# Performance work log

Measured on AMD Instinct MI355X. Metric: run time of the kernel, lower is better.

Reference implementation:

```python
import jax, jax.numpy as jnp
import numpy as np

NUM_HEADS = 16


def setup_inputs() -> dict:
    key = jax.random.key(0)
    k0, k1, k2, k3 = jax.random.split(key, 4)
    B, N, C = 8, 1024, 1024
    D = C // NUM_HEADS
    x = jax.random.normal(k0, (B, N, C), dtype=jnp.float32)
    # RoPE angle table [1, N, 1, head_dim]
    rope_freqs = jax.random.uniform(k1, (1, N, 1, D), dtype=jnp.float32) * (2.0 * jnp.pi)
    # qkv: Linear(dim, 3*dim, bias=False); proj: Linear(dim, dim) with bias
    qkv_w = jax.random.normal(k2, (3 * C, C), dtype=jnp.float32) * 0.02
    proj_w = jax.random.normal(k3, (C, C), dtype=jnp.float32) * 0.02
    proj_b = jnp.zeros((C,), dtype=jnp.float32)
    return {"x": x, "rope_freqs": rope_freqs, "qkv_w": qkv_w, "proj_w": proj_w, "proj_b": proj_b}


def _rotate_half(t):
    t1, t2 = jnp.split(t, 2, axis=-1)
    return jnp.concatenate([-t2, t1], axis=-1)


def reference(x, rope_freqs, qkv_w, proj_w, proj_b):
    B, N, C = x.shape
    H = NUM_HEADS
    D = C // H
    scale = D ** (-0.5)
    # QKV projection -> [3, B, H, N, D]
    qkv = (x @ qkv_w.T).reshape(B, N, 3, H, D).transpose(2, 0, 3, 1, 4)
    q, k, v = qkv[0], qkv[1], qkv[2]
    # RoPE: freqs [1, N, 1, D] -> [1, 1, N, D], applied to all tokens (n_special = 0)
    freqs = jnp.transpose(rope_freqs, (0, 2, 1, 3))
    cos = jnp.cos(freqs).astype(q.dtype)
    sin = jnp.sin(freqs).astype(q.dtype)
    q = q * cos + _rotate_half(q) * sin
    k = k * cos + _rotate_half(k) * sin
    # Full materialized attention (as in source)
    attn = jax.nn.softmax(jnp.einsum("bhnd,bhmd->bhnm", q, k) * scale, axis=-1)
    out = jnp.einsum("bhnm,bhmd->bhnd", attn, v)  # [B, H, N, D]
    out = out.transpose(0, 2, 1, 3).reshape(B, N, C)
    return out @ proj_w.T + proj_b
```

## Files before the change

### kernel.cpp

```cpp
#include <hip/hip_runtime.h>


typedef __attribute__((ext_vector_type(8))) short bf16x8;
typedef __attribute__((ext_vector_type(4))) float floatx4;
typedef __attribute__((ext_vector_type(4))) unsigned int u32x4;
typedef __attribute__((ext_vector_type(2))) unsigned int u32x2;

__device__ __forceinline__ void gld16(const void* g, void* l) {
  __builtin_amdgcn_global_load_lds((const __attribute__((address_space(1))) void*)g,
                                   (__attribute__((address_space(3))) void*)l, 16, 0, 0);
}

__device__ __forceinline__ short f2bf(float f) {
  unsigned u = __builtin_bit_cast(unsigned, f);
  u = (u + 0x7FFFu + ((u >> 16) & 1u)) >> 16;
  return (short)u;
}
__device__ __forceinline__ unsigned cvtpk(float lo, float hi) {
  unsigned r;
  asm("v_cvt_pk_bf16_f32 %0, %1, %2" : "=v"(r) : "v"(lo), "v"(hi));
  return r;
}
__device__ __forceinline__ float pexp(float x) {
  float r;
  asm("v_exp_f32 %0, %1" : "=v"(r) : "v"(x));
  return r;
}

__global__ __launch_bounds__(256) void prep_all(const float* __restrict__ sx,
                                                const float* __restrict__ sq,
                                                const float* __restrict__ sp,
                                                short* __restrict__ dst,
                                                const float* __restrict__ ropef,
                                                float2* __restrict__ tbl) {
  int bid = blockIdx.x;
  if (bid < 12288) {
    int i = bid * 256 + threadIdx.x;
    const float4* src;
    if (i < 2097152)      src = reinterpret_cast<const float4*>(sx) + i;
    else if (i < 2883584) src = reinterpret_cast<const float4*>(sq) + (i - 2097152);
    else                  src = reinterpret_cast<const float4*>(sp) + (i - 2883584);
    float4 v = *src;
    short4 o;
    o.x = f2bf(v.x); o.y = f2bf(v.y); o.z = f2bf(v.z); o.w = f2bf(v.w);
    reinterpret_cast<short4*>(dst)[i] = o;
  } else {
    int i = (bid - 12288) * 256 + threadIdx.x;
    float v = ropef[i];
    tbl[i] = make_float2(cosf(v), sinf(v));
  }
}

#define QSCALE 0.18033688011112042f

__device__ __forceinline__ void gemm_main(const short* __restrict__ A,
                                          const short* __restrict__ Bm,
                                          short* As, short* Bs,
                                          floatx4 (&acc)[2][4],
                                          int bx, int by) {
  const int tid = threadIdx.x;
  const int wid = tid >> 6, lane = tid & 63;
  const int g = lane >> 4, l15 = lane & 15;
  const int wr = wid >> 2, wc = wid & 3;
  const size_t trow = (size_t)by * 128, tcol = (size_t)bx * 256;
  floatx4 zero = {0.f, 0.f, 0.f, 0.f};
  #pragma unroll
  for (int i = 0; i < 2; ++i)
    #pragma unroll
    for (int j = 0; j < 4; ++j) acc[i][j] = zero;

  auto stage = [&](int buf, int k0) {
    {
      const int cb = wid * 64;
      const int c  = cb + lane;
      const int r  = c >> 3, s = c & 7;
      const int koff = k0 + ((s ^ (r & 7)) << 3);
      gld16(A + (trow + r) * 1024 + koff, As + buf * 8192 + (size_t)cb * 8);
    }
    #pragma unroll
    for (int i = 0; i < 2; ++i) {
      const int cb = (i * 16 + wid) * 64;
      const int c  = cb + lane;
      const int r  = c >> 3, s = c & 7;
      const int koff = k0 + ((s ^ (r & 7)) << 3);
      gld16(Bm + (tcol + r) * 1024 + koff, Bs + buf * 16384 + (size_t)cb * 8);
    }
  };

  stage(0, 0);
  __syncthreads();

  for (int t = 0; t < 16; ++t) {
    const int buf = t & 1;
    if (t < 15) stage(buf ^ 1, (t + 1) * 64);
    const short* Ab = As + buf * 8192;
    const short* Bb = Bs + buf * 16384;
    #pragma unroll
    for (int ks = 0; ks < 2; ++ks) {
      bf16x8 af[2], bfr[4];
      #pragma unroll
      for (int mi = 0; mi < 2; ++mi) {
        int row = wr * 32 + mi * 16 + l15;
        int ch  = (ks * 4 + g) ^ (row & 7);
        af[mi] = *reinterpret_cast<const bf16x8*>(Ab + row * 64 + ch * 8);
      }
      #pragma unroll
      for (int nt = 0; nt < 4; ++nt) {
        int row = wc * 64 + nt * 16 + l15;
        int ch  = (ks * 4 + g) ^ (row & 7);
        bfr[nt] = *reinterpret_cast<const bf16x8*>(Bb + row * 64 + ch * 8);
      }
      __builtin_amdgcn_s_setprio(1);
      #pragma unroll
      for (int mi = 0; mi < 2; ++mi)
        #pragma unroll
        for (int nt = 0; nt < 4; ++nt)
          acc[mi][nt] = __builtin_amdgcn_mfma_f32_16x16x32_bf16(af[mi], bfr[nt],
                                                                acc[mi][nt], 0, 0, 0);
      __builtin_amdgcn_s_setprio(0);
    }
    __syncthreads();
  }
}

__global__ __launch_bounds__(1024, 4) void gemm_qkv_k(const short* __restrict__ A,
                                                      const short* __restrict__ Bm,
                                                      const float2* __restrict__ tbl,
                                                      short* __restrict__ qo,
                                                      short* __restrict__ ko,
                                                      short* __restrict__ vt) {
  extern __shared__ __align__(16) short smem[];
  short* As = smem;
  short* Bs = smem + 16384;
  const int id  = blockIdx.y * 12 + blockIdx.x;
  const int sid = (id & 7) * 96 + (id >> 3);
  const int bx  = sid % 12, by = sid / 12;
  floatx4 acc[2][4];
  gemm_main(A, Bm, As, Bs, acc, bx, by);

  const int tid = threadIdx.x;
  const int wid = tid >> 6, lane = tid & 63;
  const int g = lane >> 4, l15 = lane & 15;
  const int wr = wid >> 2, wc = wid & 3;
  const int trow = by * 128, tcol = bx * 256;
  const int which = bx >> 2;

  if (which < 2) {
    short* dst = which == 0 ? qo : ko;
    const float sc = which == 0 ? QSCALE : 1.0f;
    #pragma unroll
    for (int nt = 0; nt < 2; ++nt) {
      int col = tcol + wc * 64 + nt * 16 + l15;
      int hc = col & 1023, h = hc >> 6, d1 = hc & 63;
      #pragma unroll
      for (int mi = 0; mi < 2; ++mi)
        #pragma unroll
        for (int r = 0; r < 4; ++r) {
          int rowg = trow + wr * 32 + mi * 16 + g * 4 + r;
          int b = rowg >> 10, n = rowg & 1023;
          float a1 = acc[mi][nt][r], a2 = acc[mi][nt + 2][r];
          float2 c1 = tbl[n * 64 + d1];
          float2 c2 = tbl[n * 64 + d1 + 32];
          float o1 = (a1 * c1.x - a2 * c1.y) * sc;
          float o2 = (a2 * c2.x + a1 * c2.y) * sc;
          size_t base = ((size_t)(b * 16 + h) * 1024 + n) * 64;
          dst[base + d1]      = f2bf(o1);
          dst[base + d1 + 32] = f2bf(o2);
        }
    }
  } else {
    #pragma unroll
    for (int nt = 0; nt < 4; ++nt) {
      int col = tcol + wc * 64 + nt * 16 + l15;
      int hc = col & 1023, h = hc >> 6, d = hc & 63;
      #pragma unroll
      for (int mi = 0; mi < 2; ++mi) {
        int rowg = trow + wr * 32 + mi * 16 + g * 4;
        int b = rowg >> 10, n0 = rowg & 1023;
        ushort4 pk;
        pk.x = (unsigned short)f2bf(acc[mi][nt][0]);
        pk.y = (unsigned short)f2bf(acc[mi][nt][1]);
        pk.z = (unsigned short)f2bf(acc[mi][nt][2]);
        pk.w = (unsigned short)f2bf(acc[mi][nt][3]);
        *reinterpret_cast<ushort4*>((unsigned short*)vt +
            ((size_t)(b * 16 + h) * 64 + d) * 1024 + n0) = pk;
      }
    }
  }
}

__global__ __launch_bounds__(1024, 4) void gemm_proj_k(const short* __restrict__ A,
                                                       const short* __restrict__ Bm,
                                                       const float* __restrict__ pb,
                                                       float* __restrict__ out) {
  extern __shared__ __align__(16) short smem[];
  short* As = smem;
  short* Bs = smem + 16384;
  const int id  = blockIdx.y * 4 + blockIdx.x;
  const int sid = (id & 7) * 32 + (id >> 3);
  const int bx  = sid % 4, by = sid / 4;
  floatx4 acc[2][4];
  gemm_main(A, Bm, As, Bs, acc, bx, by);

  const int tid = threadIdx.x;
  const int wid = tid >> 6, lane = tid & 63;
  const int g = lane >> 4, l15 = lane & 15;
  const int wr = wid >> 2, wc = wid & 3;
  const int trow = by * 128, tcol = bx * 256;
  #pragma unroll
  for (int nt = 0; nt < 4; ++nt) {
    int col = tcol + wc * 64 + nt * 16 + l15;
    float bias = pb[col];
    #pragma unroll
    for (int mi = 0; mi < 2; ++mi)
      #pragma unroll
      for (int r = 0; r < 4; ++r) {
        int rowg = trow + wr * 32 + mi * 16 + g * 4 + r;
        out[(size_t)rowg * 1024 + col] = acc[mi][nt][r] + bias;
      }
  }
}

__global__ __launch_bounds__(256) void attn_kernel(const short* __restrict__ qs,
                                                   const short* __restrict__ ksrc,
                                                   const short* __restrict__ vt,
                                                   short* __restrict__ aout) {
  __shared__ __align__(16) short Kl[3][64 * 64];
  __shared__ __align__(16) short Vl[3][64 * 64];

  const int tid = threadIdx.x, wid = tid >> 6, lane = tid & 63;
  const int g = lane >> 4, l15 = lane & 15;
  const int bh = blockIdx.x, q0 = blockIdx.y * 128;
  const size_t bhoff = (size_t)bh * 1024 * 64;
  const short* Kb = ksrc + bhoff;
  const short* Vb = vt + bhoff;
  const int slb = (lane & 48) + ((lane >> 4) << 2);

  const short* QpA = qs + bhoff + (size_t)(q0 + wid * 16 + l15) * 64 + g * 8;
  bf16x8 qA0 = *reinterpret_cast<const bf16x8*>(QpA);
  bf16x8 qA1 = *reinterpret_cast<const bf16x8*>(QpA + 32);
  const short* QpB = QpA + 64 * 64;
  bf16x8 qB0 = *reinterpret_cast<const bf16x8*>(QpB);
  bf16x8 qB1 = *reinterpret_cast<const bf16x8*>(QpB + 32);

  floatx4 oA[4], oB[4];
  floatx4 zero = {0.f, 0.f, 0.f, 0.f};
  #pragma unroll
  for (int i = 0; i < 4; ++i) { oA[i] = zero; oB[i] = zero; }
  float lrunA = 0.f, lrunB = 0.f;

  auto stage = [&](int buf, int t) {
    #pragma unroll
    for (int i = 0; i < 2; ++i) {
      const int cb = (i * 4 + wid) * 64;
      const int c = cb + lane;
      const int r = c >> 3, s = c & 7;
      const int off = (s ^ (r & 7)) << 3;
      gld16(Kb + (size_t)(t * 64 + r) * 64 + off, &Kl[buf][cb * 8]);
      gld16(Vb + (size_t)r * 1024 + t * 64 + off, &Vl[buf][cb * 8]);
    }
  };

#define SOFTMAX(s4, lrun, pa0, pa1)                                            \
  do {                                                                         \
    unsigned w[4][2];                                                          \
    _Pragma("unroll")                                                          \
    for (int kt = 0; kt < 4; ++kt) {                                           \
      float p0 = pexp(s4[kt][0]), p1 = pexp(s4[kt][1]);                        \
      float p2 = pexp(s4[kt][2]), p3 = pexp(s4[kt][3]);                        \
      lrun += (p0 + p1) + (p2 + p3);                                           \
      w[kt][0] = cvtpk(p0, p1);                                                \
      w[kt][1] = cvtpk(p2, p3);                                                \
    }                                                                          \
    unsigned W[2][2][2];                                                       \
    _Pragma("unroll")                                                          \
    for (int ks = 0; ks < 2; ++ks)                                             \
      _Pragma("unroll")                                                        \
      for (int h = 0; h < 2; ++h) {                                            \
        u32x2 y = __builtin_amdgcn_permlane32_swap(w[2 * ks][h],               \
                                                   w[2 * ks + 1][h],           \
                                                   false, false);              \
        u32x2 z = __builtin_amdgcn_permlane16_swap(y[0], y[1], false, false);  \
        W[ks][0][h] = z[0];                                                    \
        W[ks][1][h] = z[1];                                                    \
      }                                                                        \
    u32x4 aw0 = {W[0][0][0], W[0][0][1], W[0][1][0], W[0][1][1]};              \
    u32x4 aw1 = {W[1][0][0], W[1][0][1], W[1][1][0], W[1][1][1]};              \
    pa0 = __builtin_bit_cast(bf16x8, aw0);                                     \
    pa1 = __builtin_bit_cast(bf16x8, aw1);                                     \
  } while (0)

  stage(0, 0);
  stage(1, 1);
  asm volatile("s_waitcnt vmcnt(4)" ::: "memory");
  __builtin_amdgcn_s_barrier();
  asm volatile("" ::: "memory");

  int btop = 0;
  for (int t = 0; t < 16; ++t) {
    if (t < 14) {
      int bnx = btop + 2; if (bnx >= 3) bnx -= 3;
      stage(bnx, t + 2);
    }

    floatx4 sA[4], sB[4];
    #pragma unroll
    for (int kt = 0; kt < 4; ++kt) { sA[kt] = zero; sB[kt] = zero; }
    __builtin_amdgcn_s_setprio(1);
    #pragma unroll
    for (int kt = 0; kt < 4; ++kt) {
      int krow = kt * 16 + l15;
      int ch0 = (g ^ (krow & 7)) << 3, ch1 = ((4 + g) ^ (krow & 7)) << 3;
      bf16x8 kf0 = *reinterpret_cast<const bf16x8*>(&Kl[btop][krow * 64 + ch0]);
      sA[kt] = __builtin_amdgcn_mfma_f32_16x16x32_bf16(kf0, qA0, sA[kt], 0, 0, 0);
      sB[kt] = __builtin_amdgcn_mfma_f32_16x16x32_bf16(kf0, qB0, sB[kt], 0, 0, 0);
      bf16x8 kf1 = *reinterpret_cast<const bf16x8*>(&Kl[btop][krow * 64 + ch1]);
      sA[kt] = __builtin_amdgcn_mfma_f32_16x16x32_bf16(kf1, qA1, sA[kt], 0, 0, 0);
      sB[kt] = __builtin_amdgcn_mfma_f32_16x16x32_bf16(kf1, qB1, sB[kt], 0, 0, 0);
    }
    __builtin_amdgcn_s_setprio(0);

    bf16x8 paA0, paA1, paB0, paB1;
    SOFTMAX(sA, lrunA, paA0, paA1);
    SOFTMAX(sB, lrunB, paB0, paB1);

    __builtin_amdgcn_s_setprio(1);
    #pragma unroll
    for (int nt = 0; nt < 4; ++nt) {
      int row = nt * 16 + l15;
      int ch0 = (g ^ (row & 7)) << 3, ch1 = ((4 + g) ^ (row & 7)) << 3;
      bf16x8 vf0 = *reinterpret_cast<const bf16x8*>(&Vl[btop][row * 64 + ch0]);
      oA[nt] = __builtin_amdgcn_mfma_f32_16x16x32_bf16(paA0, vf0, oA[nt], 0, 0, 0);
      oB[nt] = __builtin_amdgcn_mfma_f32_16x16x32_bf16(paB0, vf0, oB[nt], 0, 0, 0);
      bf16x8 vf1 = *reinterpret_cast<const bf16x8*>(&Vl[btop][row * 64 + ch1]);
      oA[nt] = __builtin_amdgcn_mfma_f32_16x16x32_bf16(paA1, vf1, oA[nt], 0, 0, 0);
      oB[nt] = __builtin_amdgcn_mfma_f32_16x16x32_bf16(paB1, vf1, oB[nt], 0, 0, 0);
    }
    __builtin_amdgcn_s_setprio(0);

    if (t < 15) {
      if (t < 14) asm volatile("s_waitcnt vmcnt(4)" ::: "memory");
      else        asm volatile("s_waitcnt vmcnt(0)" ::: "memory");
      __builtin_amdgcn_s_barrier();
      asm volatile("" ::: "memory");
    }
    btop = btop + 1 == 3 ? 0 : btop + 1;
  }

  const int b = bh >> 4, h = bh & 15;
  lrunA += __shfl_xor(lrunA, 16); lrunA += __shfl_xor(lrunA, 32);
  lrunB += __shfl_xor(lrunB, 16); lrunB += __shfl_xor(lrunB, 32);
  float invA = 1.f / lrunA, invB = 1.f / lrunB;
  #pragma unroll
  for (int r = 0; r < 4; ++r) {
    float irA = __shfl(invA, slb + r);
    float irB = __shfl(invB, slb + r);
    int nA = q0 + wid * 16 + g * 4 + r;
    size_t baseA = ((size_t)(b * 1024) + nA) * 1024 + h * 64;
    size_t baseB = baseA + (size_t)64 * 1024;
    #pragma unroll
    for (int nt = 0; nt < 4; ++nt) {
      aout[baseA + nt * 16 + l15] = f2bf(oA[nt][r] * irA);
      aout[baseB + nt * 16 + l15] = f2bf(oB[nt][r] * irB);
    }
  }
#undef SOFTMAX
}

extern "C" void kernel_launch(void* const* d_in, const int* in_sizes, int n_in,
                              void* d_out, int out_size, void* d_ws, size_t ws_size,
                              hipStream_t stream) {
  const float* x      = (const float*)d_in[0];
  const float* ropef  = (const float*)d_in[1];
  const float* qkv_w  = (const float*)d_in[2];
  const float* proj_w = (const float*)d_in[3];
  const float* proj_b = (const float*)d_in[4];
  float* out = (float*)d_out;

  char* ws = (char*)d_ws;
  short*  xb  = (short*)(ws + 0);
  short*  wqb = (short*)(ws + 16777216);
  short*  wpb = (short*)(ws + 23068672);
  short*  qb  = (short*)(ws + 25165824);
  short*  kb  = (short*)(ws + 41943040);
  short*  vtb = (short*)(ws + 58720256);
  short*  aob = (short*)(ws + 75497472);
  float2* tbl = (float2*)(ws + 92274688);

  prep_all<<<12544, 256, 0, stream>>>(x, qkv_w, proj_w, xb, ropef, tbl);

  gemm_qkv_k<<<dim3(12, 64), 1024, 98304, stream>>>(xb, wqb, tbl, qb, kb, vtb);
  attn_kernel<<<dim3(128, 8), 256, 0, stream>>>(qb, kb, vtb, aob);
  gemm_proj_k<<<dim3(4, 64), 1024, 98304, stream>>>(aob, wpb, proj_b, out);
}
```

Before: 156.2 us.

## Process four query tiles per wave in attention and slice QK/softmax/PV by key half

Each attention block now covers 256 query rows instead of 128, so every wave works on four 16-row query tiles and each K/V tile staged in LDS is reused across twice as many queries. Grid size is halved. The per-tile loop is also split into two key-halves, each running QK, softmax and PV in turn, which keeps fewer score registers live despite the larger accumulator set. The aim is to cut redundant K/V global loads and LDS traffic per query. The cost is more registers per wave (sixteen output accumulators) and only 512 blocks, which may reduce occupancy and CU fill.

```diff
diff --git a/kernel.cpp b/kernel.cpp
--- a/kernel.cpp
+++ b/kernel.cpp
@@ -230,7 +230,7 @@
 
   const int tid = threadIdx.x, wid = tid >> 6, lane = tid & 63;
   const int g = lane >> 4, l15 = lane & 15;
-  const int bh = blockIdx.x, q0 = blockIdx.y * 128;
+  const int bh = blockIdx.x, q0 = blockIdx.y * 256;
   const size_t bhoff = (size_t)bh * 1024 * 64;
   const short* Kb = ksrc + bhoff;
   const short* Vb = vt + bhoff;
@@ -239,15 +239,18 @@
   const short* QpA = qs + bhoff + (size_t)(q0 + wid * 16 + l15) * 64 + g * 8;
   bf16x8 qA0 = *reinterpret_cast<const bf16x8*>(QpA);
   bf16x8 qA1 = *reinterpret_cast<const bf16x8*>(QpA + 32);
-  const short* QpB = QpA + 64 * 64;
-  bf16x8 qB0 = *reinterpret_cast<const bf16x8*>(QpB);
-  bf16x8 qB1 = *reinterpret_cast<const bf16x8*>(QpB + 32);
-
-  floatx4 oA[4], oB[4];
+  bf16x8 qB0 = *reinterpret_cast<const bf16x8*>(QpA + 64 * 64);
+  bf16x8 qB1 = *reinterpret_cast<const bf16x8*>(QpA + 64 * 64 + 32);
+  bf16x8 qC0 = *reinterpret_cast<const bf16x8*>(QpA + 128 * 64);
+  bf16x8 qC1 = *reinterpret_cast<const bf16x8*>(QpA + 128 * 64 + 32);
+  bf16x8 qD0 = *reinterpret_cast<const bf16x8*>(QpA + 192 * 64);
+  bf16x8 qD1 = *reinterpret_cast<const bf16x8*>(QpA + 192 * 64 + 32);
+
+  floatx4 oA[4], oB[4], oC[4], oD[4];
   floatx4 zero = {0.f, 0.f, 0.f, 0.f};
   #pragma unroll
-  for (int i = 0; i < 4; ++i) { oA[i] = zero; oB[i] = zero; }
-  float lrunA = 0.f, lrunB = 0.f;
+  for (int i = 0; i < 4; ++i) { oA[i] = zero; oB[i] = zero; oC[i] = zero; oD[i] = zero; }
+  float lrunA = 0.f, lrunB = 0.f, lrunC = 0.f, lrunD = 0.f;
 
   auto stage = [&](int buf, int t) {
     #pragma unroll
@@ -261,34 +264,55 @@
     }
   };
 
-#define SOFTMAX(s4, lrun, pa0, pa1)                                            \
+#define SOFTSLICE(s_, lrun, pa)                                                \
   do {                                                                         \
-    unsigned w[4][2];                                                          \
-    _Pragma("unroll")                                                          \
-    for (int kt = 0; kt < 4; ++kt) {                                           \
-      float p0 = pexp(s4[kt][0]), p1 = pexp(s4[kt][1]);                        \
-      float p2 = pexp(s4[kt][2]), p3 = pexp(s4[kt][3]);                        \
-      lrun += (p0 + p1) + (p2 + p3);                                           \
-      w[kt][0] = cvtpk(p0, p1);                                                \
-      w[kt][1] = cvtpk(p2, p3);                                                \
-    }                                                                          \
-    unsigned W[2][2][2];                                                       \
-    _Pragma("unroll")                                                          \
-    for (int ks = 0; ks < 2; ++ks)                                             \
-      _Pragma("unroll")                                                        \
-      for (int h = 0; h < 2; ++h) {                                            \
-        u32x2 y = __builtin_amdgcn_permlane32_swap(w[2 * ks][h],               \
-                                                   w[2 * ks + 1][h],           \
-                                                   false, false);              \
-        u32x2 z = __builtin_amdgcn_permlane16_swap(y[0], y[1], false, false);  \
-        W[ks][0][h] = z[0];                                                    \
-        W[ks][1][h] = z[1];                                                    \
-      }                                                                        \
-    u32x4 aw0 = {W[0][0][0], W[0][0][1], W[0][1][0], W[0][1][1]};              \
-    u32x4 aw1 = {W[1][0][0], W[1][0][1], W[1][1][0], W[1][1][1]};              \
-    pa0 = __builtin_bit_cast(bf16x8, aw0);                                     \
-    pa1 = __builtin_bit_cast(bf16x8, aw1);                                     \
+    float p0 = pexp(s_[0][0]), p1 = pexp(s_[0][1]);                            \
+    float p2 = pexp(s_[0][2]), p3 = pexp(s_[0][3]);                            \
+    float p4 = pexp(s_[1][0]), p5 = pexp(s_[1][1]);                            \
+    float p6 = pexp(s_[1][2]), p7 = pexp(s_[1][3]);                            \
+    lrun += ((p0 + p1) + (p2 + p3)) + ((p4 + p5) + (p6 + p7));                 \
+    unsigned wa0 = cvtpk(p0, p1), wa1 = cvtpk(p2, p3);                         \
+    unsigned wb0 = cvtpk(p4, p5), wb1 = cvtpk(p6, p7);                         \
+    u32x2 y0 = __builtin_amdgcn_permlane32_swap(wa0, wb0, false, false);       \
+    u32x2 z0 = __builtin_amdgcn_permlane16_swap(y0[0], y0[1], false, false);   \
+    u32x2 y1 = __builtin_amdgcn_permlane32_swap(wa1, wb1, false, false);       \
+    u32x2 z1 = __builtin_amdgcn_permlane16_swap(y1[0], y1[1], false, false);   \
+    u32x4 aw = {z0[0], z1[0], z0[1], z1[1]};                                   \
+    pa = __builtin_bit_cast(bf16x8, aw);                                       \
   } while (0)
+
+#define QKSLICE(base, sA_, sB_, sC_, sD_)                                      \
+  __builtin_amdgcn_s_setprio(1);                                               \
+  _Pragma("unroll")                                                            \
+  for (int kk = 0; kk < 2; ++kk) {                                             \
+    int krow = (base + kk) * 16 + l15;                                         \
+    int ch0 = (g ^ (krow & 7)) << 3, ch1 = ((4 + g) ^ (krow & 7)) << 3;        \
+    bf16x8 kf0 = *reinterpret_cast<const bf16x8*>(&Kl[btop][krow * 64 + ch0]); \
+    sA_[kk] = __builtin_amdgcn_mfma_f32_16x16x32_bf16(kf0, qA0, sA_[kk],0,0,0);\
+    sB_[kk] = __builtin_amdgcn_mfma_f32_16x16x32_bf16(kf0, qB0, sB_[kk],0,0,0);\
+    sC_[kk] = __builtin_amdgcn_mfma_f32_16x16x32_bf16(kf0, qC0, sC_[kk],0,0,0);\
+    sD_[kk] = __builtin_amdgcn_mfma_f32_16x16x32_bf16(kf0, qD0, sD_[kk],0,0,0);\
+    bf16x8 kf1 = *reinterpret_cast<const bf16x8*>(&Kl[btop][krow * 64 + ch1]); \
+    sA_[kk] = __builtin_amdgcn_mfma_f32_16x16x32_bf16(kf1, qA1, sA_[kk],0,0,0);\
+    sB_[kk] = __builtin_amdgcn_mfma_f32_16x16x32_bf16(kf1, qB1, sB_[kk],0,0,0);\
+    sC_[kk] = __builtin_amdgcn_mfma_f32_16x16x32_bf16(kf1, qC1, sC_[kk],0,0,0);\
+    sD_[kk] = __builtin_amdgcn_mfma_f32_16x16x32_bf16(kf1, qD1, sD_[kk],0,0,0);\
+  }                                                                            \
+  __builtin_amdgcn_s_setprio(0);
+
+#define PVSLICE(chsel, paA_, paB_, paC_, paD_)                                 \
+  __builtin_amdgcn_s_setprio(1);                                               \
+  _Pragma("unroll")                                                            \
+  for (int nt = 0; nt < 4; ++nt) {                                             \
+    int row = nt * 16 + l15;                                                   \
+    int ch = (((chsel) + g) ^ (row & 7)) << 3;                                 \
+    bf16x8 vf = *reinterpret_cast<const bf16x8*>(&Vl[btop][row * 64 + ch]);    \
+    oA[nt] = __builtin_amdgcn_mfma_f32_16x16x32_bf16(paA_, vf, oA[nt],0,0,0);  \
+    oB[nt] = __builtin_amdgcn_mfma_f32_16x16x32_bf16(paB_, vf, oB[nt],0,0,0);  \
+    oC[nt] = __builtin_amdgcn_mfma_f32_16x16x32_bf16(paC_, vf, oC[nt],0,0,0);  \
+    oD[nt] = __builtin_amdgcn_mfma_f32_16x16x32_bf16(paD_, vf, oD[nt],0,0,0);  \
+  }                                                                            \
+  __builtin_amdgcn_s_setprio(0);
 
   stage(0, 0);
   stage(1, 1);
@@ -303,40 +327,30 @@
       stage(bnx, t + 2);
     }
 
-    floatx4 sA[4], sB[4];
-    #pragma unroll
-    for (int kt = 0; kt < 4; ++kt) { sA[kt] = zero; sB[kt] = zero; }
-    __builtin_amdgcn_s_setprio(1);
-    #pragma unroll
-    for (int kt = 0; kt < 4; ++kt) {
-      int krow = kt * 16 + l15;
-      int ch0 = (g ^ (krow & 7)) << 3, ch1 = ((4 + g) ^ (krow & 7)) << 3;
-      bf16x8 kf0 = *reinterpret_cast<const bf16x8*>(&Kl[btop][krow * 64 + ch0]);
-      sA[kt] = __builtin_amdgcn_mfma_f32_16x16x32_bf16(kf0, qA0, sA[kt], 0, 0, 0);
-      sB[kt] = __builtin_amdgcn_mfma_f32_16x16x32_bf16(kf0, qB0, sB[kt], 0, 0, 0);
-      bf16x8 kf1 = *reinterpret_cast<const bf16x8*>(&Kl[btop][krow * 64 + ch1]);
-      sA[kt] = __builtin_amdgcn_mfma_f32_16x16x32_bf16(kf1, qA1, sA[kt], 0, 0, 0);
-      sB[kt] = __builtin_amdgcn_mfma_f32_16x16x32_bf16(kf1, qB1, sB[kt], 0, 0, 0);
-    }
-    __builtin_amdgcn_s_setprio(0);
-
-    bf16x8 paA0, paA1, paB0, paB1;
-    SOFTMAX(sA, lrunA, paA0, paA1);
-    SOFTMAX(sB, lrunB, paB0, paB1);
-
-    __builtin_amdgcn_s_setprio(1);
-    #pragma unroll
-    for (int nt = 0; nt < 4; ++nt) {
-      int row = nt * 16 + l15;
-      int ch0 = (g ^ (row & 7)) << 3, ch1 = ((4 + g) ^ (row & 7)) << 3;
-      bf16x8 vf0 = *reinterpret_cast<const bf16x8*>(&Vl[btop][row * 64 + ch0]);
-      oA[nt] = __builtin_amdgcn_mfma_f32_16x16x32_bf16(paA0, vf0, oA[nt], 0, 0, 0);
-      oB[nt] = __builtin_amdgcn_mfma_f32_16x16x32_bf16(paB0, vf0, oB[nt], 0, 0, 0);
-      bf16x8 vf1 = *reinterpret_cast<const bf16x8*>(&Vl[btop][row * 64 + ch1]);
-      oA[nt] = __builtin_amdgcn_mfma_f32_16x16x32_bf16(paA1, vf1, oA[nt], 0, 0, 0);
-      oB[nt] = __builtin_amdgcn_mfma_f32_16x16x32_bf16(paB1, vf1, oB[nt], 0, 0, 0);
-    }
-    __builtin_amdgcn_s_setprio(0);
+    {
+      floatx4 sA[2], sB[2], sC[2], sD[2];
+      #pragma unroll
+      for (int kk = 0; kk < 2; ++kk) { sA[kk]=zero; sB[kk]=zero; sC[kk]=zero; sD[kk]=zero; }
+      QKSLICE(0, sA, sB, sC, sD);
+      bf16x8 paA, paB, paC, paD;
+      SOFTSLICE(sA, lrunA, paA);
+      SOFTSLICE(sB, lrunB, paB);
+      SOFTSLICE(sC, lrunC, paC);
+      SOFTSLICE(sD, lrunD, paD);
+      PVSLICE(0, paA, paB, paC, paD);
+    }
+    {
+      floatx4 sA[2], sB[2], sC[2], sD[2];
+      #pragma unroll
+      for (int kk = 0; kk < 2; ++kk) { sA[kk]=zero; sB[kk]=zero; sC[kk]=zero; sD[kk]=zero; }
+      QKSLICE(2, sA, sB, sC, sD);
+      bf16x8 paA, paB, paC, paD;
+      SOFTSLICE(sA, lrunA, paA);
+      SOFTSLICE(sB, lrunB, paB);
+      SOFTSLICE(sC, lrunC, paC);
+      SOFTSLICE(sD, lrunD, paD);
+      PVSLICE(4, paA, paB, paC, paD);
+    }
 
     if (t < 15) {
       if (t < 14) asm volatile("s_waitcnt vmcnt(4)" ::: "memory");
@@ -350,21 +364,32 @@
   const int b = bh >> 4, h = bh & 15;
   lrunA += __shfl_xor(lrunA, 16); lrunA += __shfl_xor(lrunA, 32);
   lrunB += __shfl_xor(lrunB, 16); lrunB += __shfl_xor(lrunB, 32);
+  lrunC += __shfl_xor(lrunC, 16); lrunC += __shfl_xor(lrunC, 32);
+  lrunD += __shfl_xor(lrunD, 16); lrunD += __shfl_xor(lrunD, 32);
   float invA = 1.f / lrunA, invB = 1.f / lrunB;
+  float invC = 1.f / lrunC, invD = 1.f / lrunD;
   #pragma unroll
   for (int r = 0; r < 4; ++r) {
     float irA = __shfl(invA, slb + r);
     float irB = __shfl(invB, slb + r);
+    float irC = __shfl(invC, slb + r);
+    float irD = __shfl(invD, slb + r);
     int nA = q0 + wid * 16 + g * 4 + r;
     size_t baseA = ((size_t)(b * 1024) + nA) * 1024 + h * 64;
     size_t baseB = baseA + (size_t)64 * 1024;
+    size_t baseC = baseA + (size_t)128 * 1024;
+    size_t baseD = baseA + (size_t)192 * 1024;
     #pragma unroll
     for (int nt = 0; nt < 4; ++nt) {
       aout[baseA + nt * 16 + l15] = f2bf(oA[nt][r] * irA);
       aout[baseB + nt * 16 + l15] = f2bf(oB[nt][r] * irB);
-    }
-  }
-#undef SOFTMAX
+      aout[baseC + nt * 16 + l15] = f2bf(oC[nt][r] * irC);
+      aout[baseD + nt * 16 + l15] = f2bf(oD[nt][r] * irD);
+    }
+  }
+#undef SOFTSLICE
+#undef QKSLICE
+#undef PVSLICE
 }
 
 extern "C" void kernel_launch(void* const* d_in, const int* in_sizes, int n_in,
@@ -390,6 +415,6 @@
   prep_all<<<12544, 256, 0, stream>>>(x, qkv_w, proj_w, xb, ropef, tbl);
 
   gemm_qkv_k<<<dim3(12, 64), 1024, 98304, stream>>>(xb, wqb, tbl, qb, kb, vtb);
-  attn_kernel<<<dim3(128, 8), 256, 0, stream>>>(qb, kb, vtb, aob);
+  attn_kernel<<<dim3(128, 4), 256, 0, stream>>>(qb, kb, vtb, aob);
   gemm_proj_k<<<dim3(4, 64), 1024, 98304, stream>>>(aob, wpb, proj_b, out);
 }
```

Result: no change. 156.1 us (-0.0%).
